# Optimization experiments

Hardware: AMD Instinct MI355X
Metric: run time of the kernel (lower is better)

## Reference

```python
import jax, jax.numpy as jnp
import numpy as np

B, S, H, E, V, P = 64, 1024, 512, 512, 32000, 40


def setup_inputs() -> dict:
    key = jax.random.key(0)
    ks = jax.random.split(key, 18)
    s = 0.05  # weight scale to keep tanh/sigmoid in active range
    inp = {}
    inp["input_token"] = jax.random.randint(ks[0], (B,), 0, V, dtype=jnp.int32)
    inp["hidden"] = jax.random.normal(ks[1], (1, B, H), jnp.float32)
    inp["cell"] = jax.random.normal(ks[2], (1, B, H), jnp.float32)
    inp["encoder_outputs"] = jax.random.normal(ks[3], (B, S, H), jnp.float32)
    pos_ids = jax.random.randint(ks[4], (B, S), 0, P)
    inp["pos_onehot"] = jax.nn.one_hot(pos_ids, P, dtype=jnp.float32)
    inp["src_mask"] = jnp.zeros((B, S), dtype=bool)  # no PAD (avoids all -inf rows)
    # learned parameters (torch Linear convention: y = x @ W.T + b)
    inp["embed_table"] = jax.random.normal(ks[5], (V, E), jnp.float32) * s
    inp["W_s"] = jax.random.normal(ks[6], (H, H), jnp.float32) * s
    inp["W_h"] = jax.random.normal(ks[7], (H, H), jnp.float32) * s
    inp["V_w"] = jax.random.normal(ks[8], (H,), jnp.float32) * s
    inp["W_p"] = jax.random.normal(ks[9], (P,), jnp.float32) * s
    inp["b_p"] = jax.random.normal(ks[10], (), jnp.float32) * s
    inp["W_ih"] = jax.random.normal(ks[11], (4 * H, E + H), jnp.float32) * s
    inp["W_hh"] = jax.random.normal(ks[12], (4 * H, H), jnp.float32) * s
    inp["b_ih"] = jax.random.normal(ks[13], (4 * H,), jnp.float32) * s
    inp["b_hh"] = jax.random.normal(ks[14], (4 * H,), jnp.float32) * s
    inp["W_out"] = jax.random.normal(ks[15], (V, H), jnp.float32) * s
    inp["b_out"] = jax.random.normal(ks[16], (V,), jnp.float32) * s
    return inp


def reference(input_token, hidden, cell, encoder_outputs, pos_onehot, src_mask,
              embed_table, W_s, W_h, V_w, W_p, b_p,
              W_ih, W_hh, b_ih, b_hh, W_out, b_out):
    # embedding (dropout is identity in eval)
    emb = embed_table[input_token]                                  # (B, E)
    q = hidden[-1]                                                  # (B, H)
    # POS-gated Bahdanau attention
    qs = q @ W_s.T                                                  # (B, H)
    eh = jnp.einsum('bsh,kh->bsk', encoder_outputs, W_h)            # (B, S, H)
    energy = jnp.tanh(qs[:, None, :] + eh)                          # (B, S, H)
    scores = jnp.einsum('bsh,h->bs', energy, V_w)                   # (B, S)
    gate = jax.nn.sigmoid(pos_onehot @ W_p + b_p)                   # (B, S)
    gated = jnp.where(src_mask, jnp.float32(-1e30), scores * gate)
    attn = jax.nn.softmax(gated, axis=-1)                           # (B, S)
    context = jnp.einsum('bs,bsh->bh', attn, encoder_outputs)       # (B, H)
    # single-step, single-layer LSTM (torch gate order: i, f, g, o)
    lstm_in = jnp.concatenate([emb, context], axis=-1)              # (B, E+H)
    gates = lstm_in @ W_ih.T + hidden[0] @ W_hh.T + b_ih + b_hh     # (B, 4H)
    i, f, g, o = jnp.split(gates, 4, axis=-1)
    c1 = jax.nn.sigmoid(f) * cell[0] + jax.nn.sigmoid(i) * jnp.tanh(g)
    h1 = jax.nn.sigmoid(o) * jnp.tanh(c1)                           # (B, H)
    pred = h1 @ W_out.T + b_out                                     # (B, V)
    return (pred, h1[None], c1[None], attn)
```

## Files before the change

kernel.cpp:

```cpp
#include <hip/hip_runtime.h>

#define BB 64
#define SS 1024
#define HH 512
#define EE 512
#define VV 32000
#define PP 40

typedef __attribute__((ext_vector_type(8))) __bf16 bf16x8;
typedef __attribute__((ext_vector_type(4))) float f32x4;
typedef __attribute__((ext_vector_type(8))) unsigned short us8_t;
typedef __attribute__((ext_vector_type(4))) unsigned short us4_t;

__device__ inline float fast_tanh(float x) {
    float e = __expf(-2.0f * fabsf(x));
    float t = (1.0f - e) / (1.0f + e);
    return copysignf(t, x);
}
__device__ inline float sigmf(float x) { return 1.0f / (1.0f + __expf(-x)); }

__device__ inline unsigned int cvtpk(float lo, float hi) {
    unsigned int r;
    asm("v_cvt_pk_bf16_f32 %0, %1, %2" : "=v"(r) : "v"(lo), "v"(hi));
    return r;
}
__device__ inline us8_t pack8c(float4 x, float4 y) {
    union { unsigned int u[4]; us8_t v; } r;
    r.u[0] = cvtpk(x.x, x.y); r.u[1] = cvtpk(x.z, x.w);
    r.u[2] = cvtpk(y.x, y.y); r.u[3] = cvtpk(y.z, y.w);
    return r.v;
}

typedef __attribute__((address_space(1))) const unsigned char gas_t;
typedef __attribute__((address_space(3))) unsigned char las_t;
__device__ inline void gload16(const void* g, void* l) {
    __builtin_amdgcn_global_load_lds((gas_t*)g, (las_t*)l, 16, 0, 0);
}

__global__ __launch_bounds__(256)
void k_pre(const float* __restrict__ hidden, const float* __restrict__ Ws,
           const float* __restrict__ Wh, const float* __restrict__ pos,
           const float* __restrict__ Wp, const float* __restrict__ bp,
           const int* __restrict__ tok, const float* __restrict__ embt,
           unsigned short* __restrict__ wh16, float* __restrict__ qs,
           float* __restrict__ gate, float* __restrict__ ctx,
           unsigned short* __restrict__ emb16, unsigned short* __restrict__ h16v) {
    int blk = blockIdx.x, t = threadIdx.x;
    if (blk < 64) {
        __shared__ float hb[HH];
        int b = blk;
        for (int i = t; i < HH; i += 256) hb[i] = hidden[b * HH + i];
        __syncthreads();
        for (int n = t; n < HH; n += 256) {
            const float* wr = Ws + (size_t)n * HH;
            float acc = 0.0f;
#pragma unroll 4
            for (int k = 0; k < HH; k += 4) {
                float4 w = *(const float4*)(wr + k);
                acc += w.x * hb[k] + w.y * hb[k + 1] + w.z * hb[k + 2] + w.w * hb[k + 3];
            }
            qs[b * HH + n] = acc;
        }
        const float* er = embt + (size_t)tok[b] * EE;
        for (int i = 2 * t; i < HH; i += 512) {
            *(unsigned int*)(emb16 + b * 512 + i) = cvtpk(er[i], er[i + 1]);
            *(unsigned int*)(h16v + b * 512 + i) = cvtpk(hb[i], hb[i + 1]);
        }
    } else if (blk < 96) {
        int base = (blk - 64) * 8192 + t * 4;
#pragma unroll
        for (int j = 0; j < 8; ++j) {
            int idx = base + j * 1024;
            float4 x = *(const float4*)(Wh + idx);
            union { unsigned int u[2]; us4_t v; } r;
            r.u[0] = cvtpk(x.x, x.y); r.u[1] = cvtpk(x.z, x.w);
            *(us4_t*)(wh16 + idx) = r.v;
        }
    } else if (blk < 352) {
        int idx = (blk - 96) * 256 + t;
        const float* pr = pos + (size_t)idx * PP;
        float acc = bp[0];
#pragma unroll
        for (int j = 0; j < 10; ++j) {
            float4 x = *(const float4*)(pr + j * 4);
            acc += x.x * Wp[j * 4] + x.y * Wp[j * 4 + 1] + x.z * Wp[j * 4 + 2] + x.w * Wp[j * 4 + 3];
        }
        gate[idx] = sigmf(acc);
    } else {
        int idx = (blk - 352) * 256 + t;
#pragma unroll
        for (int j = 0; j < 16; ++j) ctx[idx * 16 + j] = 0.0f;
    }
}

__global__ __launch_bounds__(512)
void k_scores(const float* __restrict__ enc,
              const unsigned short* __restrict__ wh16,
              const float* __restrict__ qs, const float* __restrict__ Vw,
              float* __restrict__ part) {
    __shared__ unsigned short Abuf[2][4096];
    __shared__ unsigned short Bbuf[2][8192];
    __shared__ float pbuf[4][128];
    int bid = blockIdx.x;
    int nh = bid >> 9, rest = bid & 511;
    int b = rest >> 3, sc = rest & 7;
    int s0 = sc * 128, n0 = nh * 256;
    int tid = threadIdx.x;
    int w = tid >> 6, lane = tid & 63;
    int wm = w >> 2, wn = w & 3;
    int l15 = lane & 15, lq = lane >> 4;

    float qv[4], vw[4];
#pragma unroll
    for (int nf = 0; nf < 4; ++nf) {
        int n = n0 + wn * 64 + nf * 16 + l15;
        qv[nf] = qs[b * HH + n];
        vw[nf] = Vw[n];
    }

    int arow = tid >> 2, aseg = tid & 3;
    int akeyw = (arow >> 1) & 3;
    const float* aSrc = enc + (size_t)(b * SS + s0 + arow) * HH + aseg * 8;
    int aWr = arow * 64 + ((aseg ^ akeyw) << 4);

    unsigned int colbB = (unsigned int)((((lane & 3) ^ ((lane >> 3) & 3)) & 3) << 4);
    const char* gB0 = (const char*)(wh16 + (size_t)n0 * HH);
    int bRowS = w * 16 + (lane >> 2);
    int ldsOffB = w * 1024 + lane * 16;

    int aRdB[4], akey[4], bRdB[4], bkey[4];
#pragma unroll
    for (int mf = 0; mf < 4; ++mf) {
        int r = wm * 64 + mf * 16 + l15;
        aRdB[mf] = r * 64;
        akey[mf] = ((r >> 1) & 3) << 4;
    }
#pragma unroll
    for (int nf = 0; nf < 4; ++nf) {
        int r = wn * 64 + nf * 16 + l15;
        bRdB[nf] = r * 64;
        bkey[nf] = ((r >> 1) & 3) << 4;
    }

    f32x4 acc[4][4];
#pragma unroll
    for (int mf = 0; mf < 4; ++mf)
#pragma unroll
        for (int nf = 0; nf < 4; ++nf) acc[mf][nf] = (f32x4){0.f, 0.f, 0.f, 0.f};

#define COMPUTE(BUF)                                                            \
    {                                                                           \
        us8_t af[4], bfr[4];                                                    \
        _Pragma("unroll")                                                       \
        for (int mf = 0; mf < 4; ++mf)                                          \
            af[mf] = *(const us8_t*)((const char*)Abuf[BUF] + aRdB[mf] +        \
                                     ((lq << 4) ^ akey[mf]));                   \
        _Pragma("unroll")                                                       \
        for (int nf = 0; nf < 4; ++nf)                                          \
            bfr[nf] = *(const us8_t*)((const char*)Bbuf[BUF] + bRdB[nf] +       \
                                      ((lq << 4) ^ bkey[nf]));                  \
        _Pragma("unroll")                                                       \
        for (int mf = 0; mf < 4; ++mf)                                          \
            _Pragma("unroll")                                                   \
            for (int nf = 0; nf < 4; ++nf)                                      \
                acc[mf][nf] = __builtin_amdgcn_mfma_f32_16x16x32_bf16(          \
                    __builtin_bit_cast(bf16x8, af[mf]),                         \
                    __builtin_bit_cast(bf16x8, bfr[nf]), acc[mf][nf], 0, 0, 0); \
    }

    float4 xa0 = *(const float4*)(aSrc);
    float4 xa1 = *(const float4*)(aSrc + 4);
#pragma unroll
    for (int p = 0; p < 2; ++p)
        gload16(gB0 + (size_t)(p * 128 + bRowS) * 1024 + colbB,
                (char*)Bbuf[0] + p * 8192 + ldsOffB);
    asm volatile("s_waitcnt vmcnt(2)" ::: "memory");
    *(us8_t*)((char*)Abuf[0] + aWr) = pack8c(xa0, xa1);
    xa0 = *(const float4*)(aSrc + 32);
    xa1 = *(const float4*)(aSrc + 36);
    asm volatile("s_waitcnt vmcnt(2)" ::: "memory");
    asm volatile("s_waitcnt lgkmcnt(0)" ::: "memory");
    __builtin_amdgcn_s_barrier();

#pragma unroll
    for (int kt = 0; kt < 16; ++kt) {
        if (kt < 15) {
#pragma unroll
            for (int p = 0; p < 2; ++p)
                gload16(gB0 + (size_t)(p * 128 + bRowS) * 1024 + (kt + 1) * 64 + colbB,
                        (char*)Bbuf[(kt + 1) & 1] + p * 8192 + ldsOffB);
            asm volatile("s_waitcnt vmcnt(2)" ::: "memory");
            *(us8_t*)((char*)Abuf[(kt + 1) & 1] + aWr) = pack8c(xa0, xa1);
            if (kt < 14) {
                const float* g = aSrc + (kt + 2) * 32;
                xa0 = *(const float4*)(g);
                xa1 = *(const float4*)(g + 4);
            }
        }
        COMPUTE(kt & 1);
        if (kt < 14) {
            asm volatile("s_waitcnt vmcnt(2)" ::: "memory");
        } else if (kt == 14) {
            asm volatile("s_waitcnt vmcnt(0)" ::: "memory");
        }
        if (kt < 15) {
            asm volatile("s_waitcnt lgkmcnt(0)" ::: "memory");
            __builtin_amdgcn_s_barrier();
        }
    }
#undef COMPUTE

#pragma unroll
    for (int mf = 0; mf < 4; ++mf)
#pragma unroll
        for (int r = 0; r < 4; ++r) {
            float p = 0.0f;
#pragma unroll
            for (int nf = 0; nf < 4; ++nf)
                p += vw[nf] * fast_tanh(acc[mf][nf][r] + qv[nf]);
            p += __shfl_xor(p, 1, 64);
            p += __shfl_xor(p, 2, 64);
            p += __shfl_xor(p, 4, 64);
            p += __shfl_xor(p, 8, 64);
            if (l15 == 0) pbuf[wn][wm * 64 + mf * 16 + lq * 4 + r] = p;
        }
    __syncthreads();
    if (tid < 128) {
        part[nh * (BB * SS) + b * SS + s0 + tid] =
            pbuf[0][tid] + pbuf[1][tid] + pbuf[2][tid] + pbuf[3][tid];
    }
}

__global__ __launch_bounds__(256)
void k_context(const float* __restrict__ enc, const float* __restrict__ part,
               const float* __restrict__ gate, const unsigned char* __restrict__ mask,
               float* __restrict__ attn, float* __restrict__ ctx) {
    int b = blockIdx.x >> 4, chunk = blockIdx.x & 15;
    int s0 = chunk * 64, t = threadIdx.x;
    int w = t >> 6, ln = t & 63;
    float sum = 0.0f;
#pragma unroll
    for (int j = 0; j < 4; ++j) {
        int s = j * 256 + t;
        float raw = part[b * SS + s] + part[BB * SS + b * SS + s];
        float v = mask[b * SS + s] ? -1e30f : raw * gate[b * SS + s];
        sum += __expf(v);
    }
#pragma unroll
    for (int off = 1; off < 64; off <<= 1) sum += __shfl_xor(sum, off, 64);
    __shared__ float sl[4];
    if (ln == 0) sl[w] = sum;
    __syncthreads();
    float inv = 1.0f / (sl[0] + sl[1] + sl[2] + sl[3]);

    __shared__ float aw[64];
    if (t < 64) {
        int s = s0 + t;
        float raw = part[b * SS + s] + part[BB * SS + b * SS + s];
        float v = mask[b * SS + s] ? -1e30f : raw * gate[b * SS + s];
        float a = __expf(v) * inv;
        aw[t] = a;
        attn[b * SS + s] = a;
    }
    __syncthreads();

    const float* eb = enc + ((size_t)(b * SS + s0)) * HH + 2 * t;
    float a0 = 0.f, a1 = 0.f;
#pragma unroll 4
    for (int s = 0; s < 64; ++s) {
        float2 u = *(const float2*)(eb + (size_t)s * HH);
        a0 += aw[s] * u.x;
        a1 += aw[s] * u.y;
    }
    atomicAdd(&ctx[b * HH + 2 * t], a0);
    atomicAdd(&ctx[b * HH + 2 * t + 1], a1);
}

__global__ __launch_bounds__(256)
void k_gates(const unsigned short* __restrict__ emb16, const float* __restrict__ ctx,
             const unsigned short* __restrict__ h16v,
             const float* __restrict__ Wih, const float* __restrict__ Whh,
             float* __restrict__ gpart) {
    int nt = blockIdx.x >> 2, ksl = blockIdx.x & 3;
    int wave = threadIdx.x >> 6, lane = threadIdx.x & 63;
    int l15 = lane & 15, lq = lane >> 4, k0 = lq * 8;
    int n0w = nt * 128 + wave * 32;
    f32x4 acc[4][2];
#pragma unroll
    for (int mf = 0; mf < 4; ++mf)
#pragma unroll
        for (int nf = 0; nf < 2; ++nf) acc[mf][nf] = (f32x4){0.f, 0.f, 0.f, 0.f};

    for (int ks = 0; ks < 12; ++ks) {
        int kg = ksl * 384 + ks * 32;
        us8_t af[4];
        if (kg < 512) {
#pragma unroll
            for (int mf = 0; mf < 4; ++mf)
                af[mf] = *(const us8_t*)(emb16 + (mf * 16 + l15) * 512 + kg + k0);
        } else if (kg < 1024) {
#pragma unroll
            for (int mf = 0; mf < 4; ++mf) {
                const float* cr = ctx + (size_t)(mf * 16 + l15) * 512 + (kg - 512) + k0;
                af[mf] = pack8c(*(const float4*)cr, *(const float4*)(cr + 4));
            }
        } else {
#pragma unroll
            for (int mf = 0; mf < 4; ++mf)
                af[mf] = *(const us8_t*)(h16v + (mf * 16 + l15) * 512 + (kg - 1024) + k0);
        }
#pragma unroll
        for (int nf = 0; nf < 2; ++nf) {
            int n = n0w + nf * 16 + l15;
            us8_t bu;
            if (kg < 1024) {
                const float* wr = Wih + (size_t)n * 1024 + kg + k0;
                bu = pack8c(*(const float4*)wr, *(const float4*)(wr + 4));
            } else {
                const float* wr = Whh + (size_t)n * 512 + (kg - 1024) + k0;
                bu = pack8c(*(const float4*)wr, *(const float4*)(wr + 4));
            }
#pragma unroll
            for (int mf = 0; mf < 4; ++mf)
                acc[mf][nf] = __builtin_amdgcn_mfma_f32_16x16x32_bf16(
                    __builtin_bit_cast(bf16x8, af[mf]),
                    __builtin_bit_cast(bf16x8, bu), acc[mf][nf], 0, 0, 0);
        }
    }
#pragma unroll
    for (int mf = 0; mf < 4; ++mf)
#pragma unroll
        for (int nf = 0; nf < 2; ++nf)
#pragma unroll
            for (int r = 0; r < 4; ++r) {
                int row = mf * 16 + lq * 4 + r;
                int n = n0w + nf * 16 + l15;
                gpart[ksl * (BB * 2048) + row * 2048 + n] = acc[mf][nf][r];
            }
}

__global__ __launch_bounds__(512)
void k_lstm(const float* __restrict__ gpart, const float* __restrict__ bih,
            const float* __restrict__ bhh, const float* __restrict__ cell,
            float* __restrict__ oh, float* __restrict__ oc,
            unsigned short* __restrict__ h116) {
    int b = blockIdx.x, t = threadIdx.x;
    float gi = bih[t] + bhh[t];
    float gf = bih[512 + t] + bhh[512 + t];
    float gg = bih[1024 + t] + bhh[1024 + t];
    float go = bih[1536 + t] + bhh[1536 + t];
#pragma unroll
    for (int ksl = 0; ksl < 4; ++ksl) {
        const float* gp = gpart + ksl * (BB * 2048) + b * 2048;
        gi += gp[t];
        gf += gp[512 + t];
        gg += gp[1024 + t];
        go += gp[1536 + t];
    }
    float c0 = cell[b * HH + t];
    float c1 = sigmf(gf) * c0 + sigmf(gi) * fast_tanh(gg);
    float h1 = sigmf(go) * fast_tanh(c1);
    oh[b * HH + t] = h1;
    oc[b * HH + t] = c1;
    h116[b * HH + t] = (unsigned short)(cvtpk(h1, h1) & 0xffffu);
}

__global__ __launch_bounds__(512)
void k_pred(const unsigned short* __restrict__ h116, const float* __restrict__ Wout,
            const float* __restrict__ bout, float* __restrict__ pred) {
    int wave = threadIdx.x >> 6, lane = threadIdx.x & 63;
    int l15 = lane & 15, lq = lane >> 4, k0 = lq * 8;
    int n = blockIdx.x * 128 + wave * 16 + l15;
    f32x4 acc[4];
#pragma unroll
    for (int mf = 0; mf < 4; ++mf) acc[mf] = (f32x4){0.f, 0.f, 0.f, 0.f};
    const float* wr = Wout + (size_t)n * HH;
#pragma unroll 4
    for (int ks = 0; ks < 16; ++ks) {
        float4 x = *(const float4*)(wr + ks * 32 + k0);
        float4 y = *(const float4*)(wr + ks * 32 + k0 + 4);
        us8_t bu = pack8c(x, y);
#pragma unroll
        for (int mf = 0; mf < 4; ++mf) {
            us8_t au = *(const us8_t*)(h116 + (mf * 16 + l15) * 512 + ks * 32 + k0);
            acc[mf] = __builtin_amdgcn_mfma_f32_16x16x32_bf16(
                __builtin_bit_cast(bf16x8, au),
                __builtin_bit_cast(bf16x8, bu), acc[mf], 0, 0, 0);
        }
    }
    float bo = bout[n];
#pragma unroll
    for (int mf = 0; mf < 4; ++mf)
#pragma unroll
        for (int r = 0; r < 4; ++r) {
            int row = mf * 16 + lq * 4 + r;
            pred[(size_t)row * VV + n] = acc[mf][r] + bo;
        }
}

extern "C" void kernel_launch(void* const* d_in, const int* in_sizes, int n_in,
                              void* d_out, int out_size, void* d_ws, size_t ws_size,
                              hipStream_t stream) {
    const int* tok = (const int*)d_in[0];
    const float* hidden = (const float*)d_in[1];
    const float* cell = (const float*)d_in[2];
    const float* enc = (const float*)d_in[3];
    const float* pos = (const float*)d_in[4];
    const unsigned char* mask = (const unsigned char*)d_in[5];
    const float* embt = (const float*)d_in[6];
    const float* Ws = (const float*)d_in[7];
    const float* Wh = (const float*)d_in[8];
    const float* Vw = (const float*)d_in[9];
    const float* Wp = (const float*)d_in[10];
    const float* bp = (const float*)d_in[11];
    const float* Wih = (const float*)d_in[12];
    const float* Whh = (const float*)d_in[13];
    const float* bih = (const float*)d_in[14];
    const float* bhh = (const float*)d_in[15];
    const float* Wout = (const float*)d_in[16];
    const float* bout = (const float*)d_in[17];

    float* out = (float*)d_out;
    float* pred = out;
    float* out_h = out + 2048000;
    float* out_c = out + 2080768;
    float* attn = out + 2113536;

    char* wsb = (char*)d_ws;
    unsigned short* wh16 = (unsigned short*)(wsb);
    float* qs = (float*)(wsb + (512 << 10));
    float* gate = (float*)(wsb + (640 << 10));
    float* part = (float*)(wsb + (896 << 10));
    float* ctx = (float*)(wsb + (1408 << 10));
    unsigned short* emb16 = (unsigned short*)(wsb + (1536 << 10));
    unsigned short* h16v = (unsigned short*)(wsb + (1600 << 10));
    float* gpart = (float*)(wsb + (1664 << 10));
    unsigned short* h116 = (unsigned short*)(wsb + (3712 << 10));

    hipLaunchKernelGGL(k_pre, dim3(360), dim3(256), 0, stream,
                       hidden, Ws, Wh, pos, Wp, bp, tok, embt,
                       wh16, qs, gate, ctx, emb16, h16v);
    hipLaunchKernelGGL(k_scores, dim3(1024), dim3(512), 0, stream,
                       enc, wh16, qs, Vw, part);
    hipLaunchKernelGGL(k_context, dim3(1024), dim3(256), 0, stream,
                       enc, part, gate, mask, attn, ctx);
    hipLaunchKernelGGL(k_gates, dim3(64), dim3(256), 0, stream,
                       emb16, ctx, h16v, Wih, Whh, gpart);
    hipLaunchKernelGGL(k_lstm, dim3(64), dim3(512), 0, stream,
                       gpart, bih, bhh, cell, out_h, out_c, h116);
    hipLaunchKernelGGL(k_pred, dim3(250), dim3(512), 0, stream, h116, Wout, bout, pred);
}
```

Baseline: 183.1 us.

## Restructure score GEMM: stage full A tile in LDS, stream B from registers

The scores kernel now uses 64-row tiles with 256 threads and 2048 blocks. Each block loads the whole 64x512 encoder slice into LDS as swizzled bf16 once, then each wave streams its W_h fragments straight from global memory into registers with double buffering. This removes the per-k-step barriers and the LDS staging of B. In exchange, each W_h fragment is reloaded from global (L2) by more blocks, and the 64KB LDS footprint per block may limit occupancy.

```diff
diff --git a/kernel.cpp b/kernel.cpp
--- a/kernel.cpp
+++ b/kernel.cpp
@@ -29,12 +29,6 @@
     r.u[0] = cvtpk(x.x, x.y); r.u[1] = cvtpk(x.z, x.w);
     r.u[2] = cvtpk(y.x, y.y); r.u[3] = cvtpk(y.z, y.w);
     return r.v;
-}
-
-typedef __attribute__((address_space(1))) const unsigned char gas_t;
-typedef __attribute__((address_space(3))) unsigned char las_t;
-__device__ inline void gload16(const void* g, void* l) {
-    __builtin_amdgcn_global_load_lds((gas_t*)g, (las_t*)l, 16, 0, 0);
 }
 
 __global__ __launch_bounds__(256)
@@ -93,54 +87,49 @@
     }
 }
 
-__global__ __launch_bounds__(512)
+__global__ __launch_bounds__(256)
 void k_scores(const float* __restrict__ enc,
               const unsigned short* __restrict__ wh16,
               const float* __restrict__ qs, const float* __restrict__ Vw,
               float* __restrict__ part) {
-    __shared__ unsigned short Abuf[2][4096];
-    __shared__ unsigned short Bbuf[2][8192];
-    __shared__ float pbuf[4][128];
+    __shared__ unsigned short As[64 * 512];
+    __shared__ float pbuf[4][64];
     int bid = blockIdx.x;
-    int nh = bid >> 9, rest = bid & 511;
-    int b = rest >> 3, sc = rest & 7;
-    int s0 = sc * 128, n0 = nh * 256;
+    int nh = bid >> 10, rest = bid & 1023;
+    int b = rest >> 4, sc = rest & 15;
+    int s0 = sc * 64, n0 = nh * 256;
     int tid = threadIdx.x;
     int w = tid >> 6, lane = tid & 63;
-    int wm = w >> 2, wn = w & 3;
     int l15 = lane & 15, lq = lane >> 4;
 
     float qv[4], vw[4];
 #pragma unroll
     for (int nf = 0; nf < 4; ++nf) {
-        int n = n0 + wn * 64 + nf * 16 + l15;
+        int n = n0 + w * 64 + nf * 16 + l15;
         qv[nf] = qs[b * HH + n];
         vw[nf] = Vw[n];
     }
 
-    int arow = tid >> 2, aseg = tid & 3;
-    int akeyw = (arow >> 1) & 3;
-    const float* aSrc = enc + (size_t)(b * SS + s0 + arow) * HH + aseg * 8;
-    int aWr = arow * 64 + ((aseg ^ akeyw) << 4);
-
-    unsigned int colbB = (unsigned int)((((lane & 3) ^ ((lane >> 3) & 3)) & 3) << 4);
-    const char* gB0 = (const char*)(wh16 + (size_t)n0 * HH);
-    int bRowS = w * 16 + (lane >> 2);
-    int ldsOffB = w * 1024 + lane * 16;
-
-    int aRdB[4], akey[4], bRdB[4], bkey[4];
-#pragma unroll
-    for (int mf = 0; mf < 4; ++mf) {
-        int r = wm * 64 + mf * 16 + l15;
-        aRdB[mf] = r * 64;
-        akey[mf] = ((r >> 1) & 3) << 4;
-    }
-#pragma unroll
-    for (int nf = 0; nf < 4; ++nf) {
-        int r = wn * 64 + nf * 16 + l15;
-        bRdB[nf] = r * 64;
-        bkey[nf] = ((r >> 1) & 3) << 4;
-    }
+    {
+        int ar = tid >> 2, aj = tid & 3;
+        const float* aSrc = enc + (size_t)(b * SS + s0 + ar) * HH;
+        char* arow = (char*)(As + ar * 512);
+        int akey = (ar & 7) << 4;
+#pragma unroll
+        for (int i = 0; i < 16; ++i) {
+            int c = i * 4 + aj;
+            float4 x = *(const float4*)(aSrc + c * 8);
+            float4 y = *(const float4*)(aSrc + c * 8 + 4);
+            *(us8_t*)(arow + ((c * 16) ^ akey)) = pack8c(x, y);
+        }
+    }
+    __syncthreads();
+
+    const unsigned short* bSrc = wh16 + (size_t)(n0 + w * 64 + l15) * HH + lq * 8;
+    int aRow[4], akeyR;
+    akeyR = (l15 & 7) << 4;
+#pragma unroll
+    for (int mf = 0; mf < 4; ++mf) aRow[mf] = (mf * 16 + l15) * 1024;
 
     f32x4 acc[4][4];
 #pragma unroll
@@ -148,67 +137,32 @@
 #pragma unroll
         for (int nf = 0; nf < 4; ++nf) acc[mf][nf] = (f32x4){0.f, 0.f, 0.f, 0.f};
 
-#define COMPUTE(BUF)                                                            \
-    {                                                                           \
-        us8_t af[4], bfr[4];                                                    \
-        _Pragma("unroll")                                                       \
-        for (int mf = 0; mf < 4; ++mf)                                          \
-            af[mf] = *(const us8_t*)((const char*)Abuf[BUF] + aRdB[mf] +        \
-                                     ((lq << 4) ^ akey[mf]));                   \
-        _Pragma("unroll")                                                       \
-        for (int nf = 0; nf < 4; ++nf)                                          \
-            bfr[nf] = *(const us8_t*)((const char*)Bbuf[BUF] + bRdB[nf] +       \
-                                      ((lq << 4) ^ bkey[nf]));                  \
-        _Pragma("unroll")                                                       \
-        for (int mf = 0; mf < 4; ++mf)                                          \
-            _Pragma("unroll")                                                   \
-            for (int nf = 0; nf < 4; ++nf)                                      \
-                acc[mf][nf] = __builtin_amdgcn_mfma_f32_16x16x32_bf16(          \
-                    __builtin_bit_cast(bf16x8, af[mf]),                         \
-                    __builtin_bit_cast(bf16x8, bfr[nf]), acc[mf][nf], 0, 0, 0); \
-    }
-
-    float4 xa0 = *(const float4*)(aSrc);
-    float4 xa1 = *(const float4*)(aSrc + 4);
-#pragma unroll
-    for (int p = 0; p < 2; ++p)
-        gload16(gB0 + (size_t)(p * 128 + bRowS) * 1024 + colbB,
-                (char*)Bbuf[0] + p * 8192 + ldsOffB);
-    asm volatile("s_waitcnt vmcnt(2)" ::: "memory");
-    *(us8_t*)((char*)Abuf[0] + aWr) = pack8c(xa0, xa1);
-    xa0 = *(const float4*)(aSrc + 32);
-    xa1 = *(const float4*)(aSrc + 36);
-    asm volatile("s_waitcnt vmcnt(2)" ::: "memory");
-    asm volatile("s_waitcnt lgkmcnt(0)" ::: "memory");
-    __builtin_amdgcn_s_barrier();
+    us8_t b2[2][4];
+#pragma unroll
+    for (int nf = 0; nf < 4; ++nf)
+        b2[0][nf] = *(const us8_t*)(bSrc + (size_t)nf * 16 * HH);
 
 #pragma unroll
     for (int kt = 0; kt < 16; ++kt) {
         if (kt < 15) {
 #pragma unroll
-            for (int p = 0; p < 2; ++p)
-                gload16(gB0 + (size_t)(p * 128 + bRowS) * 1024 + (kt + 1) * 64 + colbB,
-                        (char*)Bbuf[(kt + 1) & 1] + p * 8192 + ldsOffB);
-            asm volatile("s_waitcnt vmcnt(2)" ::: "memory");
-            *(us8_t*)((char*)Abuf[(kt + 1) & 1] + aWr) = pack8c(xa0, xa1);
-            if (kt < 14) {
-                const float* g = aSrc + (kt + 2) * 32;
-                xa0 = *(const float4*)(g);
-                xa1 = *(const float4*)(g + 4);
-            }
-        }
-        COMPUTE(kt & 1);
-        if (kt < 14) {
-            asm volatile("s_waitcnt vmcnt(2)" ::: "memory");
-        } else if (kt == 14) {
-            asm volatile("s_waitcnt vmcnt(0)" ::: "memory");
-        }
-        if (kt < 15) {
-            asm volatile("s_waitcnt lgkmcnt(0)" ::: "memory");
-            __builtin_amdgcn_s_barrier();
-        }
-    }
-#undef COMPUTE
+            for (int nf = 0; nf < 4; ++nf)
+                b2[(kt + 1) & 1][nf] =
+                    *(const us8_t*)(bSrc + (size_t)nf * 16 * HH + (kt + 1) * 32);
+        }
+        us8_t af[4];
+#pragma unroll
+        for (int mf = 0; mf < 4; ++mf)
+            af[mf] = *(const us8_t*)((const char*)As + aRow[mf] +
+                                     ((kt * 64 + lq * 16) ^ akeyR));
+#pragma unroll
+        for (int mf = 0; mf < 4; ++mf)
+#pragma unroll
+            for (int nf = 0; nf < 4; ++nf)
+                acc[mf][nf] = __builtin_amdgcn_mfma_f32_16x16x32_bf16(
+                    __builtin_bit_cast(bf16x8, af[mf]),
+                    __builtin_bit_cast(bf16x8, b2[kt & 1][nf]), acc[mf][nf], 0, 0, 0);
+    }
 
 #pragma unroll
     for (int mf = 0; mf < 4; ++mf)
@@ -222,10 +176,10 @@
             p += __shfl_xor(p, 2, 64);
             p += __shfl_xor(p, 4, 64);
             p += __shfl_xor(p, 8, 64);
-            if (l15 == 0) pbuf[wn][wm * 64 + mf * 16 + lq * 4 + r] = p;
+            if (l15 == 0) pbuf[w][mf * 16 + lq * 4 + r] = p;
         }
     __syncthreads();
-    if (tid < 128) {
+    if (tid < 64) {
         part[nh * (BB * SS) + b * SS + s0 + tid] =
             pbuf[0][tid] + pbuf[1][tid] + pbuf[2][tid] + pbuf[3][tid];
     }
@@ -440,7 +394,7 @@
     hipLaunchKernelGGL(k_pre, dim3(360), dim3(256), 0, stream,
                        hidden, Ws, Wh, pos, Wp, bp, tok, embt,
                        wh16, qs, gate, ctx, emb16, h16v);
-    hipLaunchKernelGGL(k_scores, dim3(1024), dim3(512), 0, stream,
+    hipLaunchKernelGGL(k_scores, dim3(2048), dim3(256), 0, stream,
                        enc, wh16, qs, Vw, part);
     hipLaunchKernelGGL(k_context, dim3(1024), dim3(256), 0, stream,
                        enc, part, gate, mask, attn, ctx);
```

Measured after the change: 204.8 us. 11.9% more time.
